# Kernel tuning notes

Hardware: AMD Instinct MI355X
Metric: run time of the kernel (lower is better)

The kernel has to match this reference:

```python
import jax, jax.numpy as jnp
import numpy as np

SEQ = 4096
BLOCK = 64
NUM_RAND = 3
B, H, D = 1, 12, 64


def _build_bigbird_mask(seq_len=SEQ, block=BLOCK, num_rand=NUM_RAND, seed=0):
    """Dense [S,S] BigBird mask: global first/last block, window +-1 block,
    num_rand random blocks per middle row (mirrors bigbird_block_rand_mask)."""
    nb = seq_len // block
    rng = np.random.RandomState(seed)
    m = np.zeros((nb, nb), dtype=np.int32)
    # global blocks (first & last block attend/are attended everywhere)
    m[0, :] = 1
    m[-1, :] = 1
    m[:, 0] = 1
    m[:, -1] = 1
    # sliding window of one block on each side
    idx = np.arange(nb)
    win = np.abs(idx[:, None] - idx[None, :]) <= 1
    m[win] = 1
    # random blocks for middle rows, excluding window and global columns
    for i in range(1, nb - 1):
        cand = np.array([j for j in range(1, nb - 1) if abs(j - i) > 1], dtype=np.int32)
        sel = rng.permutation(cand)[:num_rand]
        m[i, sel] = 1
    return np.kron(m, np.ones((block, block), dtype=np.int32))


def setup_inputs() -> dict:
    key = jax.random.key(0)
    kq, kk, kv = jax.random.split(key, 3)
    q = jax.random.normal(kq, (B, H, SEQ, D), dtype=jnp.float32)
    k = jax.random.normal(kk, (B, H, SEQ, D), dtype=jnp.float32)
    v = jax.random.normal(kv, (B, H, SEQ, D), dtype=jnp.float32)
    mask = jnp.asarray(_build_bigbird_mask(), dtype=jnp.int32)  # [S, S]
    return {"q": q, "k": k, "v": v, "mask": mask}


def reference(q, k, v, mask):
    # OriginalFullAttention with dense BigBird mask:
    # scores = QK^T / sqrt(D); masked positions get -10000 additive bias.
    scale = 1.0 / np.sqrt(D).astype(np.float32)
    scores = jnp.einsum("bhqd,bhkd->bhqk", q, k) * scale
    adder = (1.0 - mask.astype(scores.dtype)) * jnp.asarray(-10000.0, scores.dtype)
    probs = jax.nn.softmax(scores + adder[None, None, :, :], axis=-1)
    out = jnp.einsum("bhqk,bhkd->bhqd", probs, v)  # [B, H, S, D]
    return out
```

## Files before the change

### kernel.cpp

```cpp
#include <hip/hip_runtime.h>
#include <stdint.h>

#define SEQ 4096
#define DH  64
#define NB  64
#define NH  12

typedef float  f32x4   __attribute__((ext_vector_type(4)));
typedef float  f32x16  __attribute__((ext_vector_type(16)));
typedef short  s16x8   __attribute__((ext_vector_type(8)));
typedef unsigned short ushort_t;
typedef unsigned long long u64;

__device__ __forceinline__ unsigned short f2bf(float x){
    union { float f; unsigned u; } c; c.f = x;
    unsigned u = c.u;
    u += 0x7fffu + ((u >> 16) & 1u);
    return (unsigned short)(u >> 16);
}

__device__ __forceinline__ unsigned pk2(float lo, float hi){
    return (unsigned)f2bf(lo) | ((unsigned)f2bf(hi) << 16);
}

__device__ __forceinline__ s16x8 pack8(f32x4 a, f32x4 b){
    s16x8 r;
#pragma unroll
    for (int i = 0; i < 4; ++i) { r[i] = (short)f2bf(a[i]); r[i+4] = (short)f2bf(b[i]); }
    return r;
}

__device__ __forceinline__ int swz(int row, int col){
    return row * 64 + (col ^ ((row & 7) << 3));
}

#define GLOAD_LDS(gp, lp) __builtin_amdgcn_global_load_lds( \
    (const __attribute__((address_space(1))) unsigned int*)(gp), \
    (__attribute__((address_space(3))) unsigned int*)(lp), 16, 0, 0)

#define KBF_OFF   0
#define VTB_OFF   6291456
#define PART_OFF  12582912
#define BMP_OFF   15777792
#define WS_NEED   15778304
#define SLOT_F    4160

__global__ __launch_bounds__(256) void bb_conv(
        const float* __restrict__ k, const float* __restrict__ v,
        const int* __restrict__ mask,
        ushort_t* __restrict__ kbf, ushort_t* __restrict__ vtb,
        u64* __restrict__ bmp)
{
    const int kb = blockIdx.x, h = blockIdx.y;
    const int tid = threadIdx.x;
    __shared__ float vls[64*65];

    if (h == 0 && tid < 64){
        bool a = mask[(size_t)(kb*64)*SEQ + tid*64] != 0;
        u64 bm = __ballot(a);
        if (tid == 0) bmp[kb] = bm;
    }

    const int j = tid >> 2, c = (tid & 3) * 16;
    const size_t gsrc = (size_t)h*SEQ*DH + (size_t)(kb*64 + j)*DH + c;
    const size_t tdst = ((size_t)h*NB + kb) * 4096;

    {
        f32x4 a0 = *(const f32x4*)(k + gsrc);
        f32x4 a1 = *(const f32x4*)(k + gsrc + 4);
        f32x4 a2 = *(const f32x4*)(k + gsrc + 8);
        f32x4 a3 = *(const f32x4*)(k + gsrc + 12);
        *(s16x8*)&kbf[tdst + swz(j, c    )] = pack8(a0, a1);
        *(s16x8*)&kbf[tdst + swz(j, c + 8)] = pack8(a2, a3);
    }
    {
        f32x4 b0 = *(const f32x4*)(v + gsrc);
        f32x4 b1 = *(const f32x4*)(v + gsrc + 4);
        f32x4 b2 = *(const f32x4*)(v + gsrc + 8);
        f32x4 b3 = *(const f32x4*)(v + gsrc + 12);
#pragma unroll
        for (int i = 0; i < 4; ++i){
            vls[j*65 + c + i     ] = b0[i];
            vls[j*65 + c + 4 + i ] = b1[i];
            vls[j*65 + c + 8 + i ] = b2[i];
            vls[j*65 + c + 12 + i] = b3[i];
        }
    }
    __syncthreads();
    {
        const int d = tid >> 2, jc = (tid & 3) * 16;
        s16x8 r0, r1;
#pragma unroll
        for (int i = 0; i < 8; ++i){
            r0[i] = (short)f2bf(vls[(jc + i    )*65 + d]);
            r1[i] = (short)f2bf(vls[(jc + i + 8)*65 + d]);
        }
        *(s16x8*)&vtb[tdst + swz(d, jc    )] = r0;
        *(s16x8*)&vtb[tdst + swz(d, jc + 8)] = r1;
    }
}

__global__ __launch_bounds__(256) void bb_main(
        const float* __restrict__ q,
        const ushort_t* __restrict__ kbf, const ushort_t* __restrict__ vtb,
        const u64* __restrict__ bmp,
        float* __restrict__ out, float* __restrict__ part)
{
    const int lin = blockIdx.x;
    const int job = (lin & 7) * 117 + (lin >> 3);
    const int h   = job / 78;
    const int x   = job - h * 78;

    int qb, wq = -1, sp = 0; u64 rmask;
    if (x < 62) { qb = x + 1; rmask = ~0ull; }
    else { int e = x - 62; wq = e >> 3; sp = e & 7; qb = wq ? 63 : 0; rmask = 0xFFull << (sp*8); }

    const int tid  = threadIdx.x;
    const int wave = tid >> 6;
    const int lane = tid & 63;
    const int l31  = lane & 31;
    const int hi   = lane >> 5;
    const int qh   = wave >> 1;
    const int kh   = wave & 1;

    __shared__ __align__(16) ushort_t KV[2][2][4096];
    __shared__ float lsm[64];

    const size_t hoff = (size_t)h * SEQ * DH;

    s16x8 qf[4];
    {
        const float* qp = q + hoff + (size_t)(qb*64 + qh*32 + l31) * DH + 8*hi;
#pragma unroll
        for (int c = 0; c < 4; ++c){
            f32x4 a = *(const f32x4*)(qp + c*16);
            f32x4 b = *(const f32x4*)(qp + c*16 + 4);
            a *= 0.125f; b *= 0.125f;
            qf[c] = pack8(a, b);
        }
    }

    u64 bits = bmp[qb] & rmask;

    const ushort_t* Kb = kbf + (size_t)h * (NB*4096);
    const ushort_t* Vb = vtb + (size_t)h * (NB*4096);

    f32x16 oa0 = {0.f}, oa1 = {0.f};
    float lp = 0.f;

    const int soff = wave*1024 + lane*16;
#define STAGE(gbase, lbase)                                          \
    {                                                                \
        const char* g0 = (const char*)(gbase) + soff;                \
        char*       l0 = (char*)(lbase) + wave*1024;                 \
        GLOAD_LDS(g0, l0);                                           \
        GLOAD_LDS(g0 + 4096, l0 + 4096);                             \
    }

    if (bits){
        int kb = __builtin_ctzll(bits); bits &= bits - 1;
        STAGE(Kb + (size_t)kb*4096, &KV[0][0][0]);
        STAGE(Vb + (size_t)kb*4096, &KV[0][1][0]);
        __syncthreads();
        int cur = 0;
        for (;;){
            const bool more = (bits != 0);
            if (more){
                int nkb = __builtin_ctzll(bits); bits &= bits - 1;
                STAGE(Kb + (size_t)nkb*4096, &KV[cur^1][0][0]);
                STAGE(Vb + (size_t)nkb*4096, &KV[cur^1][1][0]);
            }

            const ushort_t* Kt = &KV[cur][0][0];
            const ushort_t* Vt = &KV[cur][1][0];

            f32x16 sa = {0.f};
#pragma unroll
            for (int c = 0; c < 4; ++c){
                s16x8 kf = *(const s16x8*)&Kt[swz(kh*32 + l31, c*16 + 8*hi)];
                sa = __builtin_amdgcn_mfma_f32_32x32x16_bf16(kf, qf[c], sa, 0, 0, 0);
            }

            float p[16];
#pragma unroll
            for (int r = 0; r < 16; ++r){
                p[r] = __expf(sa[r]);
                lp += p[r];
            }

            s16x8 pa[2];
#pragma unroll
            for (int s = 0; s < 2; ++s){
                unsigned a1 = pk2(p[8*s+0], p[8*s+1]);
                unsigned b1 = pk2(p[8*s+4], p[8*s+5]);
                unsigned a2 = pk2(p[8*s+2], p[8*s+3]);
                unsigned b2 = pk2(p[8*s+6], p[8*s+7]);
                asm("v_permlane32_swap_b32 %0, %1" : "+v"(a1), "+v"(b1));
                asm("v_permlane32_swap_b32 %0, %1" : "+v"(a2), "+v"(b2));
                union { unsigned w[4]; s16x8 v; } u;
                u.w[0] = a1; u.w[1] = a2; u.w[2] = b1; u.w[3] = b2;
                pa[s] = u.v;
            }

#pragma unroll
            for (int s = 0; s < 2; ++s){
                s16x8 v0 = *(const s16x8*)&Vt[swz(     l31, kh*32 + s*16 + 8*hi)];
                s16x8 v1 = *(const s16x8*)&Vt[swz(32 + l31, kh*32 + s*16 + 8*hi)];
                oa0 = __builtin_amdgcn_mfma_f32_32x32x16_bf16(pa[s], v0, oa0, 0, 0, 0);
                oa1 = __builtin_amdgcn_mfma_f32_32x32x16_bf16(pa[s], v1, oa1, 0, 0, 0);
            }

            if (!more) break;
            __syncthreads();
            cur ^= 1;
        }
    }
#undef STAGE

    float lpf = lp + __shfl_xor(lp, 32);

    __syncthreads();
    float* msm = (float*)&KV[0][0][0];

    if (kh == 1){
#pragma unroll
        for (int r = 0; r < 16; ++r){
            const int cr = (r&3) + 8*(r>>2) + 4*hi;
            msm[(qh*32 + cr)*64 +      l31] = oa0[r];
            msm[(qh*32 + cr)*64 + 32 + l31] = oa1[r];
        }
        if (lane < 32) lsm[qh*32 + lane] = lpf;
    }
    __syncthreads();

    if (kh == 0){
        const float lt = lpf + lsm[qh*32 + l31];
        if (wq < 0){
            const float inv = lt > 0.f ? 1.0f / lt : 0.f;
            float* op = out + hoff + (size_t)(qb*64 + qh*32) * DH;
#pragma unroll
            for (int r = 0; r < 16; ++r){
                const int cr = (r&3) + 8*(r>>2) + 4*hi;
                const float ir = __shfl(inv, cr);
                op[(size_t)cr*DH +      l31] = (oa0[r] + msm[(qh*32 + cr)*64 +      l31]) * ir;
                op[(size_t)cr*DH + 32 + l31] = (oa1[r] + msm[(qh*32 + cr)*64 + 32 + l31]) * ir;
            }
        } else {
            float* pp = part + ((size_t)(h*2 + wq)*8 + sp) * SLOT_F;
#pragma unroll
            for (int r = 0; r < 16; ++r){
                const int cr = (r&3) + 8*(r>>2) + 4*hi;
                pp[(qh*32 + cr)*64 +      l31] = oa0[r] + msm[(qh*32 + cr)*64 +      l31];
                pp[(qh*32 + cr)*64 + 32 + l31] = oa1[r] + msm[(qh*32 + cr)*64 + 32 + l31];
            }
            if (lane < 32) pp[4096 + qh*32 + lane] = lt;
        }
    }
}

__global__ __launch_bounds__(256) void bb_comb(
        const float* __restrict__ part, float* __restrict__ out)
{
    const int h = blockIdx.x >> 1, wq = blockIdx.x & 1;
    const int qb = wq ? 63 : 0;
    const int tid = threadIdx.x;
    const int i = tid >> 2, cg = (tid & 3) * 16;

    const float* base = part + (size_t)(h*2 + wq) * 8 * SLOT_F;
    f32x4 acc[4] = {{0,0,0,0},{0,0,0,0},{0,0,0,0},{0,0,0,0}};
    float ls = 0.f;
#pragma unroll
    for (int s = 0; s < 8; ++s){
        const float* p = base + (size_t)s * SLOT_F;
#pragma unroll
        for (int c4 = 0; c4 < 4; ++c4)
            acc[c4] += *(const f32x4*)(p + (size_t)i*DH + cg + c4*4);
        ls += p[4096 + i];
    }
    const float inv = ls > 0.f ? 1.0f / ls : 0.f;
    float* op = out + (size_t)h*SEQ*DH + (size_t)(qb*64 + i)*DH + cg;
#pragma unroll
    for (int c4 = 0; c4 < 4; ++c4){
        f32x4 r = acc[c4] * inv;
        *(f32x4*)(op + c4*4) = r;
    }
}

__global__ __launch_bounds__(256) void bb_attn_fb(
        const float* __restrict__ q, const float* __restrict__ k,
        const float* __restrict__ v, const int* __restrict__ mask,
        float* __restrict__ out)
{
    const int qb   = blockIdx.x;
    const int h    = blockIdx.y;
    const int tid  = threadIdx.x;
    const int wave = tid >> 6;
    const int lane = tid & 63;
    const int lrow = lane & 15;
    const int lgrp = lane >> 4;

    __shared__ __align__(16) ushort_t Kb[64*64];
    __shared__ __align__(16) ushort_t Vt[64*64];
    __shared__ __align__(16) ushort_t Pw[4][16*64];

    const size_t hoff = (size_t)h * SEQ * DH;
    const int qrow = qb*64 + wave*16 + lrow;
    const float* qp = q + hoff + (size_t)qrow * DH + lgrp*8;
    s16x8 qf[2];
#pragma unroll
    for (int kc = 0; kc < 2; ++kc){
        f32x4 a = *(const f32x4*)(qp + kc*32);
        f32x4 b = *(const f32x4*)(qp + kc*32 + 4);
        a *= 0.125f; b *= 0.125f;
        qf[kc] = pack8(a, b);
    }
    const f32x4 zero = {0.f,0.f,0.f,0.f};
    f32x4 oa[4] = {zero, zero, zero, zero};
    float m_run[4] = {-1e30f,-1e30f,-1e30f,-1e30f};
    float l_run[4] = {0.f,0.f,0.f,0.f};
    const int* mrow = mask + (size_t)(qb*64) * SEQ;
    const int kr  = tid >> 2, kcg  = tid & 3;
    const int j2  = tid >> 3, dgrp = tid & 7;

    for (int kb = 0; kb < NB; ++kb){
        if (mrow[kb*64] == 0) continue;
        __syncthreads();
        {
            const float* kp = k + hoff + (size_t)(kb*64 + kr) * DH + kcg*16;
            f32x4 a0 = *(const f32x4*)(kp);
            f32x4 a1 = *(const f32x4*)(kp+4);
            f32x4 a2 = *(const f32x4*)(kp+8);
            f32x4 a3 = *(const f32x4*)(kp+12);
            *(s16x8*)&Kb[(kr*64) + (kcg*16     ^ ((kr&7)<<3))] = pack8(a0, a1);
            *(s16x8*)&Kb[(kr*64) + ((kcg*16+8) ^ ((kr&7)<<3))] = pack8(a2, a3);
        }
        {
            const float* vp0 = v + hoff + (size_t)(kb*64 + 2*j2) * DH + dgrp*8;
            f32x4 b0 = *(const f32x4*)(vp0);
            f32x4 b1 = *(const f32x4*)(vp0+4);
            f32x4 b2 = *(const f32x4*)(vp0+DH);
            f32x4 b3 = *(const f32x4*)(vp0+DH+4);
            float r0[8] = {b0[0],b0[1],b0[2],b0[3],b1[0],b1[1],b1[2],b1[3]};
            float r1[8] = {b2[0],b2[1],b2[2],b2[3],b3[0],b3[1],b3[2],b3[3]};
#pragma unroll
            for (int i = 0; i < 8; ++i){
                int dd = (i + dgrp) & 7;
                int d  = dgrp*8 + dd;
                unsigned val = (unsigned)f2bf(r0[dd]) | ((unsigned)f2bf(r1[dd]) << 16);
                *(unsigned*)&Vt[(d*64) + (2*j2 ^ ((d&7)<<3))] = val;
            }
        }
        __syncthreads();
        f32x4 sa[4] = {zero, zero, zero, zero};
#pragma unroll
        for (int jt = 0; jt < 4; ++jt)
#pragma unroll
            for (int kc = 0; kc < 2; ++kc){
                int row = jt*16 + lrow, col = kc*32 + lgrp*8;
                s16x8 kf = *(const s16x8*)&Kb[row*64 + (col ^ ((row&7)<<3))];
                sa[jt] = __builtin_amdgcn_mfma_f32_16x16x32_bf16(qf[kc], kf, sa[jt], 0, 0, 0);
            }
        float fac[4];
#pragma unroll
        for (int r = 0; r < 4; ++r){
            float mx = fmaxf(fmaxf(sa[0][r], sa[1][r]), fmaxf(sa[2][r], sa[3][r]));
            mx = fmaxf(mx, __shfl_xor(mx, 1));
            mx = fmaxf(mx, __shfl_xor(mx, 2));
            mx = fmaxf(mx, __shfl_xor(mx, 4));
            mx = fmaxf(mx, __shfl_xor(mx, 8));
            float mn = fmaxf(m_run[r], mx);
            fac[r] = __expf(m_run[r] - mn);
            m_run[r] = mn;
        }
#pragma unroll
        for (int r = 0; r < 4; ++r){
            float p0 = __expf(sa[0][r] - m_run[r]);
            float p1 = __expf(sa[1][r] - m_run[r]);
            float p2 = __expf(sa[2][r] - m_run[r]);
            float p3 = __expf(sa[3][r] - m_run[r]);
            sa[0][r]=p0; sa[1][r]=p1; sa[2][r]=p2; sa[3][r]=p3;
            float sm = p0+p1+p2+p3;
            sm += __shfl_xor(sm, 1);
            sm += __shfl_xor(sm, 2);
            sm += __shfl_xor(sm, 4);
            sm += __shfl_xor(sm, 8);
            l_run[r] = l_run[r]*fac[r] + sm;
        }
#pragma unroll
        for (int dc = 0; dc < 4; ++dc)
#pragma unroll
            for (int r = 0; r < 4; ++r) oa[dc][r] *= fac[r];
#pragma unroll
        for (int jt = 0; jt < 4; ++jt)
#pragma unroll
            for (int r = 0; r < 4; ++r){
                int row = lgrp*4 + r, col = jt*16 + lrow;
                Pw[wave][row*64 + (col ^ ((row&7)<<3))] = f2bf(sa[jt][r]);
            }
        s16x8 pf0 = *(const s16x8*)&Pw[wave][lrow*64 + ((     lgrp*8) ^ ((lrow&7)<<3))];
        s16x8 pf1 = *(const s16x8*)&Pw[wave][lrow*64 + ((32 + lgrp*8) ^ ((lrow&7)<<3))];
#pragma unroll
        for (int dc = 0; dc < 4; ++dc){
            int row0 = dc*16 + lrow;
            s16x8 v0 = *(const s16x8*)&Vt[row0*64 + ((     lgrp*8) ^ ((row0&7)<<3))];
            s16x8 v1 = *(const s16x8*)&Vt[row0*64 + ((32 + lgrp*8) ^ ((row0&7)<<3))];
            oa[dc] = __builtin_amdgcn_mfma_f32_16x16x32_bf16(pf0, v0, oa[dc], 0, 0, 0);
            oa[dc] = __builtin_amdgcn_mfma_f32_16x16x32_bf16(pf1, v1, oa[dc], 0, 0, 0);
        }
    }
    float inv[4];
#pragma unroll
    for (int r = 0; r < 4; ++r) inv[r] = 1.0f / l_run[r];
    float* op = out + hoff + (size_t)(qb*64 + wave*16) * DH;
#pragma unroll
    for (int dc = 0; dc < 4; ++dc)
#pragma unroll
        for (int r = 0; r < 4; ++r)
            op[(size_t)(lgrp*4 + r) * DH + dc*16 + lrow] = oa[dc][r] * inv[r];
}

extern "C" void kernel_launch(void* const* d_in, const int* in_sizes, int n_in,
                              void* d_out, int out_size, void* d_ws, size_t ws_size,
                              hipStream_t stream)
{
    const float* q    = (const float*)d_in[0];
    const float* k    = (const float*)d_in[1];
    const float* v    = (const float*)d_in[2];
    const int*   mask = (const int*)d_in[3];
    float* out = (float*)d_out;

    if (ws_size < (size_t)WS_NEED){
        dim3 grid(NB, NH, 1);
        bb_attn_fb<<<grid, 256, 0, stream>>>(q, k, v, mask, out);
        return;
    }

    char* ws = (char*)d_ws;
    ushort_t* kbf = (ushort_t*)(ws + KBF_OFF);
    ushort_t* vtb = (ushort_t*)(ws + VTB_OFF);
    float*    prt = (float*)   (ws + PART_OFF);
    u64*      bmp = (u64*)     (ws + BMP_OFF);

    bb_conv<<<dim3(NB, NH, 1), 256, 0, stream>>>(k, v, mask, kbf, vtb, bmp);
    bb_main<<<dim3(936, 1, 1), 256, 0, stream>>>(q, kbf, vtb, bmp, out, prt);
    bb_comb<<<dim3(24, 1, 1), 256, 0, stream>>>(prt, out);
}
```

Before: 42.46 us.

## Triple-buffer K/V staging with vmcnt waits, fold log2e into Q scale

Replaces the double-buffered K/V staging loop with a three-deep ring buffer. Prefetches are issued two blocks ahead and gated by an explicit s_waitcnt vmcnt plus a single barrier per iteration. The softmax exponent now uses the native exp2 with log2(e) folded into the Q prescale, and s_setprio is raised around the MFMA sections. This costs more LDS (which can lower occupancy) and issues dummy loads of block 0 at the tail of the ring. It also relies on the vmcnt count matching exactly the number of outstanding loads per stage.

```diff
diff --git a/kernel.cpp b/kernel.cpp
--- a/kernel.cpp
+++ b/kernel.cpp
@@ -123,19 +123,20 @@
     const int qh   = wave >> 1;
     const int kh   = wave & 1;
 
-    __shared__ __align__(16) ushort_t KV[2][2][4096];
+    __shared__ __align__(16) ushort_t KV[3][2][4096];
     __shared__ float lsm[64];
 
     const size_t hoff = (size_t)h * SEQ * DH;
 
     s16x8 qf[4];
     {
+        const float sc = 0.125f * 1.4426950408889634f;
         const float* qp = q + hoff + (size_t)(qb*64 + qh*32 + l31) * DH + 8*hi;
 #pragma unroll
         for (int c = 0; c < 4; ++c){
             f32x4 a = *(const f32x4*)(qp + c*16);
             f32x4 b = *(const f32x4*)(qp + c*16 + 4);
-            a *= 0.125f; b *= 0.125f;
+            a *= sc; b *= sc;
             qf[c] = pack8(a, b);
         }
     }
@@ -158,33 +159,46 @@
     }
 
     if (bits){
-        int kb = __builtin_ctzll(bits); bits &= bits - 1;
-        STAGE(Kb + (size_t)kb*4096, &KV[0][0][0]);
-        STAGE(Vb + (size_t)kb*4096, &KV[0][1][0]);
-        __syncthreads();
-        int cur = 0;
-        for (;;){
-            const bool more = (bits != 0);
-            if (more){
-                int nkb = __builtin_ctzll(bits); bits &= bits - 1;
-                STAGE(Kb + (size_t)nkb*4096, &KV[cur^1][0][0]);
-                STAGE(Vb + (size_t)nkb*4096, &KV[cur^1][1][0]);
-            }
-
-            const ushort_t* Kt = &KV[cur][0][0];
-            const ushort_t* Vt = &KV[cur][1][0];
+        const int n = __popcll(bits);
+        u64 bpre = bits;
+
+        int kb0 = __builtin_ctzll(bpre); bpre &= bpre - 1;
+        STAGE(Kb + (size_t)kb0*4096, &KV[0][0][0]);
+        STAGE(Vb + (size_t)kb0*4096, &KV[0][1][0]);
+        int kb1 = 0;
+        if (bpre){ kb1 = __builtin_ctzll(bpre); bpre &= bpre - 1; }
+        STAGE(Kb + (size_t)kb1*4096, &KV[1][0][0]);
+        STAGE(Vb + (size_t)kb1*4096, &KV[1][1][0]);
+
+        int buf = 0;
+        for (int t = 0; t < n; ++t){
+            asm volatile("s_waitcnt vmcnt(4)" ::: "memory");
+            __builtin_amdgcn_s_barrier();
+
+            {
+                int kbn = 0;
+                if (bpre){ kbn = __builtin_ctzll(bpre); bpre &= bpre - 1; }
+                int b2 = buf + 2; if (b2 >= 3) b2 -= 3;
+                STAGE(Kb + (size_t)kbn*4096, &KV[b2][0][0]);
+                STAGE(Vb + (size_t)kbn*4096, &KV[b2][1][0]);
+            }
+
+            const ushort_t* Kt = &KV[buf][0][0];
+            const ushort_t* Vt = &KV[buf][1][0];
 
             f32x16 sa = {0.f};
+            __builtin_amdgcn_s_setprio(1);
 #pragma unroll
             for (int c = 0; c < 4; ++c){
                 s16x8 kf = *(const s16x8*)&Kt[swz(kh*32 + l31, c*16 + 8*hi)];
                 sa = __builtin_amdgcn_mfma_f32_32x32x16_bf16(kf, qf[c], sa, 0, 0, 0);
             }
+            __builtin_amdgcn_s_setprio(0);
 
             float p[16];
 #pragma unroll
             for (int r = 0; r < 16; ++r){
-                p[r] = __expf(sa[r]);
+                p[r] = __builtin_amdgcn_exp2f(sa[r]);
                 lp += p[r];
             }
 
@@ -202,6 +216,7 @@
                 pa[s] = u.v;
             }
 
+            __builtin_amdgcn_s_setprio(1);
 #pragma unroll
             for (int s = 0; s < 2; ++s){
                 s16x8 v0 = *(const s16x8*)&Vt[swz(     l31, kh*32 + s*16 + 8*hi)];
@@ -209,10 +224,9 @@
                 oa0 = __builtin_amdgcn_mfma_f32_32x32x16_bf16(pa[s], v0, oa0, 0, 0, 0);
                 oa1 = __builtin_amdgcn_mfma_f32_32x32x16_bf16(pa[s], v1, oa1, 0, 0, 0);
             }
-
-            if (!more) break;
-            __syncthreads();
-            cur ^= 1;
+            __builtin_amdgcn_s_setprio(0);
+
+            ++buf; if (buf >= 3) buf -= 3;
         }
     }
 #undef STAGE
```

After: 40.58 us. 1.05x faster.
